# Kernel tuning notes

Hardware: AMD Instinct MI355X
Metric: run time of the kernel (lower is better)

Reference implementation:

```python
import jax, jax.numpy as jnp
import numpy as np

PEAK_W = 2.0
HIGH_W = 1.0
OVERALL_W = 0.5
HIGH_RATIO = 0.8
NEG = -1e30  # sentinel for masked max (avoids -inf -> nan in grads)


def setup_inputs() -> dict:
    key = jax.random.key(0)
    k1, k2, k3 = jax.random.split(key, 3)
    B, S = 2048, 8192
    predictions = jax.random.normal(k1, (B, S, 1), dtype=jnp.float32)
    targets = jax.random.normal(k2, (B, S, 1), dtype=jnp.float32)
    flood_mask = jax.random.randint(k3, (B, S, 1), 0, 2, dtype=jnp.int32)
    return {"predictions": predictions, "targets": targets, "flood_mask": flood_mask}


def _safe_rmse(sum_sq, n):
    # sqrt(mean) with zero-count guard that is safe under autodiff
    nz = n > 0
    ms = sum_sq / jnp.maximum(n, 1).astype(sum_sq.dtype)
    return jnp.where(nz, jnp.sqrt(jnp.where(nz, ms, 1.0)), 0.0)


def reference(predictions, targets, flood_mask):
    p = predictions[:, :, 0]            # [B, S]
    t = targets[:, :, 0]                # [B, S]
    m = flood_mask[:, :, 0].astype(bool)
    valid = m & ~jnp.isnan(p) & ~jnp.isnan(t)          # flood & finite
    n = valid.sum(axis=1)                               # [B]
    nz = n > 0

    sq = jnp.where(valid, (p - t) ** 2, 0.0)
    overall_rmse = _safe_rmse(sq.sum(axis=1), n)

    t_peak = jnp.max(jnp.where(valid, t, NEG), axis=1)  # [B]
    p_peak = jnp.max(jnp.where(valid, p, NEG), axis=1)
    peak_error = jnp.where(nz, jnp.abs(p_peak - t_peak), 0.0)

    # high-value region: targ >= target_peak * high_ratio (all valid if peak <= 0)
    thr = t_peak * HIGH_RATIO
    high = valid & jnp.where((t_peak <= 0)[:, None], True, t >= thr[:, None])
    nh = high.sum(axis=1)
    high_rmse = _safe_rmse(jnp.where(high, (p - t) ** 2, 0.0).sum(axis=1), nh)

    loss = OVERALL_W * overall_rmse + PEAK_W * peak_error + HIGH_W * high_rmse  # [B]
    return jnp.mean(loss)  # reduction='mean'
```

## Files before the change

### kernel.cpp

```cpp
#include <hip/hip_runtime.h>
#include <math.h>


#define S_LEN 8192
#define BLK   1024
#define NWAVE (BLK / 64)

__device__ __forceinline__ float waveSum(float x) {
    #pragma unroll
    for (int o = 32; o > 0; o >>= 1) x += __shfl_down(x, o, 64);
    return x;
}
__device__ __forceinline__ float waveMax(float x) {
    #pragma unroll
    for (int o = 32; o > 0; o >>= 1) x = fmaxf(x, __shfl_down(x, o, 64));
    return x;
}

__global__ __launch_bounds__(BLK) void flood_loss_row(
    const float* __restrict__ P, const float* __restrict__ T,
    const int* __restrict__ M, float* __restrict__ partial)
{
    __shared__ float red1[NWAVE][4];
    __shared__ float red2[NWAVE][2];

    const int tid  = threadIdx.x;
    const int wid  = tid >> 6;
    const int lane = tid & 63;
    const size_t base = (size_t)blockIdx.x * S_LEN;

    const float4* __restrict__ P4 = (const float4*)(P + base);
    const float4* __restrict__ T4 = (const float4*)(T + base);
    const int4*   __restrict__ M4 = (const int4*)(M + base);

    float4 p0 = P4[tid];
    float4 p1 = P4[BLK + tid];
    float4 t0 = T4[tid];
    float4 t1 = T4[BLK + tid];
    int4   m0 = M4[tid];
    int4   m1 = M4[BLK + tid];

    float pe[8] = {p0.x, p0.y, p0.z, p0.w, p1.x, p1.y, p1.z, p1.w};
    float te[8] = {t0.x, t0.y, t0.z, t0.w, t1.x, t1.y, t1.z, t1.w};
    int   me[8] = {m0.x, m0.y, m0.z, m0.w, m1.x, m1.y, m1.z, m1.w};

    float tenc[8];
    float d2v [8];
    float ssq = 0.f, fn = 0.f;
    float tpk = -INFINITY, ppk = -INFINITY;

    #pragma unroll
    for (int j = 0; j < 8; ++j) {
        bool valid = (me[j] != 0) && !(pe[j] != pe[j]) && !(te[j] != te[j]);
        float d  = pe[j] - te[j];
        float d2 = valid ? d * d : 0.f;
        ssq += d2;
        fn  += valid ? 1.f : 0.f;
        if (valid) { tpk = fmaxf(tpk, te[j]); ppk = fmaxf(ppk, pe[j]); }
        tenc[j] = valid ? te[j] : -INFINITY;
        d2v [j] = d2;
    }
    asm volatile("" : "+v"(tenc[0]), "+v"(tenc[1]), "+v"(tenc[2]), "+v"(tenc[3]),
                      "+v"(tenc[4]), "+v"(tenc[5]), "+v"(tenc[6]), "+v"(tenc[7]),
                      "+v"(d2v[0]), "+v"(d2v[1]), "+v"(d2v[2]), "+v"(d2v[3]),
                      "+v"(d2v[4]), "+v"(d2v[5]), "+v"(d2v[6]), "+v"(d2v[7]));

    ssq = waveSum(ssq); fn = waveSum(fn);
    tpk = waveMax(tpk); ppk = waveMax(ppk);
    if (lane == 0) { red1[wid][0] = fn; red1[wid][1] = ssq; red1[wid][2] = tpk; red1[wid][3] = ppk; }
    __syncthreads();

    float fnT = 0.f, ssqT = 0.f, tpkT = -INFINITY, ppkT = -INFINITY;
    #pragma unroll
    for (int w = 0; w < NWAVE; ++w) {
        fnT  += red1[w][0];
        ssqT += red1[w][1];
        tpkT  = fmaxf(tpkT, red1[w][2]);
        ppkT  = fmaxf(ppkT, red1[w][3]);
    }

    const bool  tpos = tpkT > 0.f;
    const float thr  = tpkT * 0.8f;
    float nh = 0.f, ssqh = 0.f;
    #pragma unroll
    for (int k = 0; k < 8; ++k) {
        bool hi = tpos ? (tenc[k] >= thr) : (tenc[k] > -INFINITY);
        nh   += hi ? 1.f : 0.f;
        ssqh += hi ? d2v[k] : 0.f;
    }
    nh = waveSum(nh); ssqh = waveSum(ssqh);
    if (lane == 0) { red2[wid][0] = nh; red2[wid][1] = ssqh; }
    __syncthreads();

    if (tid == 0) {
        float nht = 0.f, ssqht = 0.f;
        #pragma unroll
        for (int w = 0; w < NWAVE; ++w) { nht += red2[w][0]; ssqht += red2[w][1]; }
        float overall = (fnT > 0.f) ? sqrtf(ssqT  / fmaxf(fnT, 1.f)) : 0.f;
        float high_r  = (nht > 0.f) ? sqrtf(ssqht / fmaxf(nht, 1.f)) : 0.f;
        float peak_e  = (fnT > 0.f) ? fabsf(ppkT - tpkT) : 0.f;
        partial[blockIdx.x] = 0.5f * overall + 2.0f * peak_e + 1.0f * high_r;
    }
}

__global__ __launch_bounds__(256) void bw_probe(
    const float4* __restrict__ P4, const float4* __restrict__ T4,
    const int4* __restrict__ M4, float* __restrict__ sink, int n4)
{
    float acc = 0.f;
    const int stride = gridDim.x * 256;
    for (int i = blockIdx.x * 256 + threadIdx.x; i < n4; i += stride) {
        float4 a = P4[i];
        float4 b = T4[i];
        int4   m = M4[i];
        acc += a.x + a.y + a.z + a.w + b.x + b.y + b.z + b.w
             + (float)(m.x + m.y + m.z + m.w);
    }
    acc = waveSum(acc);
    if ((threadIdx.x & 63) == 0) sink[blockIdx.x * 4 + (threadIdx.x >> 6)] = acc;
}

__global__ __launch_bounds__(1024) void flood_loss_reduce(
    const float* __restrict__ partial, float* __restrict__ out, float invB)
{
    __shared__ float s[16];
    const int tid  = threadIdx.x;
    const int wid  = tid >> 6;
    const int lane = tid & 63;
    float x = partial[tid] + partial[tid + 1024];
    x = waveSum(x);
    if (lane == 0) s[wid] = x;
    __syncthreads();
    if (tid == 0) {
        float tot = 0.f;
        #pragma unroll
        for (int w = 0; w < 16; ++w) tot += s[w];
        out[0] = tot * invB;
    }
}

extern "C" void kernel_launch(void* const* d_in, const int* in_sizes, int n_in,
                              void* d_out, int out_size, void* d_ws, size_t ws_size,
                              hipStream_t stream) {
    const float* P = (const float*)d_in[0];
    const float* T = (const float*)d_in[1];
    const int*   M = (const int*)d_in[2];
    float* out = (float*)d_out;
    float* partial = (float*)d_ws;
    float* sink    = (float*)d_ws + 4096;
    const int B = in_sizes[0] / S_LEN;
    const int n4 = in_sizes[0] / 4;

    flood_loss_row<<<B, BLK, 0, stream>>>(P, T, M, partial);
    flood_loss_reduce<<<1, 1024, 0, stream>>>(partial, out, 1.0f / (float)B);
    if (ws_size >= (4096 + 8192) * sizeof(float)) {
        bw_probe<<<2048, 256, 0, stream>>>((const float4*)P, (const float4*)T,
                                           (const int4*)M, sink, n4);
    }
}
```

Baseline: 228.7 us.

## Shrink row blocks to 256 threads, reload row in second pass, drop probe

The row kernel now uses 256-thread blocks, and each thread loops over 8 float4 chunks instead of holding 8 elements in registers. The high-region pass re-reads P, T and M from memory (likely L2-resident) rather than keeping cached values in registers. The extra bandwidth probe kernel, which read all inputs a second time, is removed. The trade-offs are a second read of each row against smaller blocks and less register pressure, and removing the probe cuts a full extra pass over the 200 MB of input.

```diff
diff --git a/kernel.cpp b/kernel.cpp
--- a/kernel.cpp
+++ b/kernel.cpp
@@ -3,8 +3,9 @@
 
 
 #define S_LEN 8192
-#define BLK   1024
+#define BLK   256
 #define NWAVE (BLK / 64)
+#define NIT   (S_LEN / 4 / BLK)
 
 __device__ __forceinline__ float waveSum(float x) {
     #pragma unroll
@@ -17,7 +18,7 @@
     return x;
 }
 
-__global__ __launch_bounds__(BLK) void flood_loss_row(
+__global__ __launch_bounds__(BLK) void flood_loss2(
     const float* __restrict__ P, const float* __restrict__ T,
     const int* __restrict__ M, float* __restrict__ partial)
 {
@@ -33,37 +34,27 @@
     const float4* __restrict__ T4 = (const float4*)(T + base);
     const int4*   __restrict__ M4 = (const int4*)(M + base);
 
-    float4 p0 = P4[tid];
-    float4 p1 = P4[BLK + tid];
-    float4 t0 = T4[tid];
-    float4 t1 = T4[BLK + tid];
-    int4   m0 = M4[tid];
-    int4   m1 = M4[BLK + tid];
-
-    float pe[8] = {p0.x, p0.y, p0.z, p0.w, p1.x, p1.y, p1.z, p1.w};
-    float te[8] = {t0.x, t0.y, t0.z, t0.w, t1.x, t1.y, t1.z, t1.w};
-    int   me[8] = {m0.x, m0.y, m0.z, m0.w, m1.x, m1.y, m1.z, m1.w};
-
-    float tenc[8];
-    float d2v [8];
     float ssq = 0.f, fn = 0.f;
     float tpk = -INFINITY, ppk = -INFINITY;
 
     #pragma unroll
-    for (int j = 0; j < 8; ++j) {
-        bool valid = (me[j] != 0) && !(pe[j] != pe[j]) && !(te[j] != te[j]);
-        float d  = pe[j] - te[j];
-        float d2 = valid ? d * d : 0.f;
-        ssq += d2;
-        fn  += valid ? 1.f : 0.f;
-        if (valid) { tpk = fmaxf(tpk, te[j]); ppk = fmaxf(ppk, pe[j]); }
-        tenc[j] = valid ? te[j] : -INFINITY;
-        d2v [j] = d2;
+    for (int it = 0; it < NIT; ++it) {
+        const int v = it * BLK + tid;
+        float4 p4 = P4[v];
+        float4 t4 = T4[v];
+        int4   m4 = M4[v];
+        float pe[4] = {p4.x, p4.y, p4.z, p4.w};
+        float te[4] = {t4.x, t4.y, t4.z, t4.w};
+        int   me[4] = {m4.x, m4.y, m4.z, m4.w};
+        #pragma unroll
+        for (int j = 0; j < 4; ++j) {
+            bool valid = (me[j] != 0) && !(pe[j] != pe[j]) && !(te[j] != te[j]);
+            float d = pe[j] - te[j];
+            ssq += valid ? d * d : 0.f;
+            fn  += valid ? 1.f : 0.f;
+            if (valid) { tpk = fmaxf(tpk, te[j]); ppk = fmaxf(ppk, pe[j]); }
+        }
     }
-    asm volatile("" : "+v"(tenc[0]), "+v"(tenc[1]), "+v"(tenc[2]), "+v"(tenc[3]),
-                      "+v"(tenc[4]), "+v"(tenc[5]), "+v"(tenc[6]), "+v"(tenc[7]),
-                      "+v"(d2v[0]), "+v"(d2v[1]), "+v"(d2v[2]), "+v"(d2v[3]),
-                      "+v"(d2v[4]), "+v"(d2v[5]), "+v"(d2v[6]), "+v"(d2v[7]));
 
     ssq = waveSum(ssq); fn = waveSum(fn);
     tpk = waveMax(tpk); ppk = waveMax(ppk);
@@ -82,12 +73,26 @@
     const bool  tpos = tpkT > 0.f;
     const float thr  = tpkT * 0.8f;
     float nh = 0.f, ssqh = 0.f;
+
     #pragma unroll
-    for (int k = 0; k < 8; ++k) {
-        bool hi = tpos ? (tenc[k] >= thr) : (tenc[k] > -INFINITY);
-        nh   += hi ? 1.f : 0.f;
-        ssqh += hi ? d2v[k] : 0.f;
+    for (int it = 0; it < NIT; ++it) {
+        const int v = it * BLK + tid;
+        float4 p4 = P4[v];
+        float4 t4 = T4[v];
+        int4   m4 = M4[v];
+        float pe[4] = {p4.x, p4.y, p4.z, p4.w};
+        float te[4] = {t4.x, t4.y, t4.z, t4.w};
+        int   me[4] = {m4.x, m4.y, m4.z, m4.w};
+        #pragma unroll
+        for (int j = 0; j < 4; ++j) {
+            bool valid = (me[j] != 0) && !(pe[j] != pe[j]) && !(te[j] != te[j]);
+            bool hi = valid && (!tpos || te[j] >= thr);
+            float d = pe[j] - te[j];
+            nh   += hi ? 1.f : 0.f;
+            ssqh += hi ? d * d : 0.f;
+        }
     }
+
     nh = waveSum(nh); ssqh = waveSum(ssqh);
     if (lane == 0) { red2[wid][0] = nh; red2[wid][1] = ssqh; }
     __syncthreads();
@@ -101,23 +106,6 @@
         float peak_e  = (fnT > 0.f) ? fabsf(ppkT - tpkT) : 0.f;
         partial[blockIdx.x] = 0.5f * overall + 2.0f * peak_e + 1.0f * high_r;
     }
-}
-
-__global__ __launch_bounds__(256) void bw_probe(
-    const float4* __restrict__ P4, const float4* __restrict__ T4,
-    const int4* __restrict__ M4, float* __restrict__ sink, int n4)
-{
-    float acc = 0.f;
-    const int stride = gridDim.x * 256;
-    for (int i = blockIdx.x * 256 + threadIdx.x; i < n4; i += stride) {
-        float4 a = P4[i];
-        float4 b = T4[i];
-        int4   m = M4[i];
-        acc += a.x + a.y + a.z + a.w + b.x + b.y + b.z + b.w
-             + (float)(m.x + m.y + m.z + m.w);
-    }
-    acc = waveSum(acc);
-    if ((threadIdx.x & 63) == 0) sink[blockIdx.x * 4 + (threadIdx.x >> 6)] = acc;
 }
 
 __global__ __launch_bounds__(1024) void flood_loss_reduce(
@@ -147,14 +135,8 @@
     const int*   M = (const int*)d_in[2];
     float* out = (float*)d_out;
     float* partial = (float*)d_ws;
-    float* sink    = (float*)d_ws + 4096;
     const int B = in_sizes[0] / S_LEN;
-    const int n4 = in_sizes[0] / 4;
 
-    flood_loss_row<<<B, BLK, 0, stream>>>(P, T, M, partial);
+    flood_loss2<<<B, BLK, 0, stream>>>(P, T, M, partial);
     flood_loss_reduce<<<1, 1024, 0, stream>>>(partial, out, 1.0f / (float)B);
-    if (ws_size >= (4096 + 8192) * sizeof(float)) {
-        bw_probe<<<2048, 256, 0, stream>>>((const float4*)P, (const float4*)T,
-                                           (const int4*)M, sink, n4);
-    }
 }
```

New measurement: 205.4 us. -10.2%, faster.
